# Performance work log

Hardware: AMD Instinct MI355X
Metric: run time of the kernel (lower is better)

The kernel has to match this reference:

```python
import jax, jax.numpy as jnp
import numpy as np

B, C, T = 8, 256, 16000
N_HALF = 32  # d_state // 2 complex modes (S4D stores conjugate pairs)
EPS = 1e-8


def setup_inputs() -> dict:
    key = jax.random.key(0)
    ks = jax.random.split(key, 8)
    x = jax.random.normal(ks[0], (B, C, T), jnp.float32)
    # ChannelwiseLayerNorm params
    gamma = jnp.ones((C,), jnp.float32)
    beta = jnp.zeros((C,), jnp.float32)
    # PReLU per-channel slope (torch default init 0.25)
    prelu_w = jnp.full((C,), 0.25, jnp.float32)
    # S4D kernel params (standard S4D init)
    log_dt = (jax.random.uniform(ks[1], (C,), jnp.float32)
              * (np.log(0.1) - np.log(0.001)) + np.log(0.001)).astype(jnp.float32)
    log_A_real = jnp.log(0.5 * jnp.ones((C, N_HALF), jnp.float32))
    A_imag = jnp.broadcast_to(np.pi * jnp.arange(N_HALF, dtype=jnp.float32), (C, N_HALF))
    C_re = jax.random.normal(ks[2], (C, N_HALF), jnp.float32) * (0.5 ** 0.5)
    C_im = jax.random.normal(ks[3], (C, N_HALF), jnp.float32) * (0.5 ** 0.5)
    D = jax.random.normal(ks[4], (C,), jnp.float32)
    # output 1x1 conv (C -> 2C) followed by GLU over channel dim
    W_out = jax.random.normal(ks[5], (2 * C, C), jnp.float32) * (1.0 / np.sqrt(C))
    b_out = jnp.zeros((2 * C,), jnp.float32)
    return dict(x=x, gamma=gamma, beta=beta, prelu_w=prelu_w, log_dt=log_dt,
                log_A_real=log_A_real, A_imag=A_imag, C_re=C_re, C_im=C_im,
                D=D, W_out=W_out, b_out=b_out)


def reference(x, gamma, beta, prelu_w, log_dt, log_A_real, A_imag, C_re, C_im, D, W_out, b_out):
    # --- channel-wise LayerNorm over C (per timestep), x: [B, C, T] ---
    mean = jnp.mean(x, axis=1, keepdims=True)
    var = jnp.mean((x - mean) ** 2, axis=1, keepdims=True)
    y = (x - mean) * jax.lax.rsqrt(var + EPS)
    y = y * gamma[None, :, None] + beta[None, :, None]
    # --- PReLU (per-channel slope) ---
    y = jnp.where(y >= 0, y, prelu_w[None, :, None] * y)
    # --- S4D convolution kernel via Vandermonde (ZOH discretization) ---
    L = x.shape[-1]
    dt = jnp.exp(log_dt)[:, None]                      # [C, 1]
    A = -jnp.exp(log_A_real) + 1j * A_imag             # [C, N]
    dtA = dt * A                                       # [C, N]
    Cc = (C_re + 1j * C_im) * (jnp.exp(dtA) - 1.0) / A  # [C, N]
    vand = jnp.exp(dtA[:, :, None] * jnp.arange(L))    # [C, N, L]
    k = 2.0 * jnp.real(jnp.einsum('hn,hnl->hl', Cc, vand))  # [C, L]
    # --- FFT-based causal convolution ---
    n = 2 * L
    y_f = jnp.fft.rfft(y, n=n)                         # [B, C, n/2+1]
    k_f = jnp.fft.rfft(k, n=n)                         # [C, n/2+1]
    s = jnp.fft.irfft(y_f * k_f[None], n=n)[..., :L]   # [B, C, T]
    s = s + y * D[None, :, None]                       # skip connection
    # --- GELU + 1x1 conv + GLU over channels ---
    s = jax.nn.gelu(s, approximate=False)
    z = jnp.einsum('bct,oc->bot', s, W_out) + b_out[None, :, None]  # [B, 2C, T]
    out = z[:, :C] * jax.nn.sigmoid(z[:, C:])
    # --- residual ---
    return x + out
```

## Files before the change

### kernel.cpp

```cpp
#include <hip/hip_runtime.h>
#include <cstdint>
#include <cstddef>

constexpr int cB = 8, cC = 256, cT = 16000, cN = 32;
constexpr int cP = 125;
constexpr float cEPS = 1e-8f;

typedef __bf16 bf16;
typedef __bf16 bf16x4 __attribute__((ext_vector_type(4)));
typedef __bf16 bf16x8 __attribute__((ext_vector_type(8)));
typedef float floatx4 __attribute__((ext_vector_type(4)));

constexpr size_t kMean = 0;
constexpr size_t kRstd = kMean + (size_t)cB * cT * 4;
constexpr size_t kWlr  = kRstd + (size_t)cB * cT * 4;
constexpr size_t kWli  = kWlr + (size_t)cC * cN * 4;
constexpr size_t kWb   = kWli + (size_t)cC * cN * 4;
constexpr size_t kLt   = kWb  + (size_t)512 * 256 * 2;
constexpr size_t kEt   = kLt  + (size_t)cC * 128 * 128 * 2;
constexpr size_t kVt   = kEt  + (size_t)cC * 64 * 128 * 2;
constexpr size_t kU    = kVt  + (size_t)cC * 128 * 64 * 2;

__device__ __forceinline__ float fast_sigmoid(float z) {
  return __builtin_amdgcn_rcpf(1.f + __builtin_amdgcn_exp2f(-z * 1.4426950408889634f));
}

__global__ void prepW_kernel(const float* __restrict__ W_out, bf16* __restrict__ Wb) {
  int idx = blockIdx.x * 256 + threadIdx.x;
  if (idx < 512 * 256) Wb[idx] = (bf16)W_out[idx];
}

__global__ void prep2_kernel(const float* __restrict__ log_dt,
                             const float* __restrict__ log_A_real,
                             const float* __restrict__ A_imag,
                             const float* __restrict__ C_re,
                             const float* __restrict__ C_im,
                             float* __restrict__ wlr, float* __restrict__ wli,
                             bf16* __restrict__ Lt, bf16* __restrict__ Et,
                             bf16* __restrict__ Vt) {
  int c = blockIdx.x;
  int j = threadIdx.x;
  __shared__ float kv[128];
  float dt = expf(log_dt[c]);
  float kj = 0.f;
  for (int n = 0; n < cN; ++n) {
    int idx = c * cN + n;
    float Ar = -expf(log_A_real[idx]);
    float Ai = A_imag[idx];
    float ar = dt * Ar, ai = dt * Ai;
    float mg = expf(ar), cw, sw;
    sincosf(ai, &sw, &cw);
    float wre = mg * cw, wim = mg * sw;
    float den = Ar * Ar + Ai * Ai;
    float emr = wre - 1.f, emi = wim;
    float qr = (emr * Ar + emi * Ai) / den;
    float qi = (emi * Ar - emr * Ai) / den;
    float cre = C_re[idx], cim = C_im[idx];
    float c2r = 2.f * (cre * qr - cim * qi);
    float c2i = 2.f * (cre * qi + cim * qr);
    float mj = expf((float)j * ar), cj, sj;
    sincosf((float)j * ai, &sj, &cj);
    float wjr = mj * cj, wji = mj * sj;
    kj += c2r * wjr - c2i * wji;
    float w1r = wjr * wre - wji * wim;
    float w1i = wjr * wim + wji * wre;
    Vt[(size_t)c * 8192 + j * 64 + 2 * n]     = (bf16)(c2r * w1r - c2i * w1i);
    Vt[(size_t)c * 8192 + j * 64 + 2 * n + 1] = (bf16)(-(c2r * w1i + c2i * w1r));
    float mr = expf((float)(127 - j) * ar), cr2, sr2;
    sincosf((float)(127 - j) * ai, &sr2, &cr2);
    Et[(size_t)c * 8192 + (2 * n) * 128 + j]     = (bf16)(mr * cr2);
    Et[(size_t)c * 8192 + (2 * n + 1) * 128 + j] = (bf16)(mr * sr2);
  }
  kv[j] = kj;
  if (j < cN) {
    int idx = c * cN + j;
    float Ar = -expf(log_A_real[idx]);
    float ai = dt * A_imag[idx], ar = dt * Ar;
    float m = expf(128.f * ar), cc, ss;
    sincosf(128.f * ai, &ss, &cc);
    wlr[idx] = m * cc;
    wli[idx] = m * ss;
  }
  __syncthreads();
  bf16* LtC = Lt + (size_t)c * 16384;
  for (int e = j; e < 4096; e += 128) {
    int t4 = e * 4;
    int row = t4 >> 7, col = t4 & 127;
    bf16x4 v;
#pragma unroll
    for (int q = 0; q < 4; ++q) {
      int ii = col + q;
      v[q] = (ii <= row) ? (bf16)kv[row - ii] : (bf16)0.f;
    }
    *(bf16x4*)(LtC + row * 128 + col) = v;
  }
}

__global__ __launch_bounds__(512)
void stats_kernel(const float* __restrict__ x,
                  float* __restrict__ meanp, float* __restrict__ rstdp) {
  __shared__ float S1[8][128], S2[8][128];
  int g0 = blockIdx.x * 128;
  int b = g0 / cT;
  int t0 = g0 - b * cT;
  int tp = threadIdx.x & 63, cq = threadIdx.x >> 6;
  const float2* xp = (const float2*)(x + ((size_t)b * cC + cq * 32) * cT + t0) + tp;
  float s1x = 0.f, s1y = 0.f, s2x = 0.f, s2y = 0.f;
#pragma unroll 8
  for (int cc = 0; cc < 32; ++cc) {
    float2 v = xp[(size_t)cc * (cT / 2)];
    s1x += v.x; s2x = fmaf(v.x, v.x, s2x);
    s1y += v.y; s2y = fmaf(v.y, v.y, s2y);
  }
  S1[cq][2 * tp] = s1x; S1[cq][2 * tp + 1] = s1y;
  S2[cq][2 * tp] = s2x; S2[cq][2 * tp + 1] = s2y;
  __syncthreads();
  if (threadIdx.x < 128) {
    float a1 = 0.f, a2 = 0.f;
#pragma unroll
    for (int q = 0; q < 8; ++q) { a1 += S1[q][threadIdx.x]; a2 += S2[q][threadIdx.x]; }
    float mean = a1 * (1.0f / cC);
    float var = fmaf(a2, 1.0f / cC, -mean * mean);
    int g = g0 + threadIdx.x;
    meanp[g] = mean;
    rstdp[g] = rsqrtf(var + cEPS);
  }
}

__global__ __launch_bounds__(512, 4)
void scanM_kernel(const float* __restrict__ x, const float* __restrict__ meanp,
                  const float* __restrict__ rstdp, const float* __restrict__ gam,
                  const float* __restrict__ bet, const float* __restrict__ prw,
                  const float* __restrict__ Dp,
                  const float* __restrict__ wlr, const float* __restrict__ wli,
                  const bf16* __restrict__ Lt, const bf16* __restrict__ Et,
                  const bf16* __restrict__ Vt, bf16* __restrict__ U) {
  __shared__ __align__(16) bf16 Y[128 * 136];
  __shared__ __align__(16) bf16 H[128 * 136];
  __shared__ float Sseg[8][32][2];

  int blk = blockIdx.x;
  int logical = (blk & 7) * 256 + (blk >> 3);
  int b = logical & 7, c = logical >> 3;
  int tid = threadIdx.x;
  int lane = tid & 63, w8 = tid >> 6, quad = lane >> 4, mh = lane & 15;
  float gamma = gam[c], beta = bet[c], pw = prw[c], Dc = Dp[c];

  const float4* x4 = (const float4*)(x + (size_t)(b * cC + c) * cT);
  const float4* m4 = (const float4*)(meanp + (size_t)b * cT);
  const float4* r4 = (const float4*)(rstdp + (size_t)b * cT);
#pragma unroll
  for (int it = 0; it < 8; ++it) {
    int i4 = tid + it * 512;
    if (i4 < 4000) {
      float4 xv = x4[i4], mv = m4[i4], rv = r4[i4];
      int t = i4 * 4, p = t >> 7, j = t & 127;
      float ys[4];
      ys[0] = fmaf((xv.x - mv.x) * rv.x, gamma, beta);
      ys[1] = fmaf((xv.y - mv.y) * rv.y, gamma, beta);
      ys[2] = fmaf((xv.z - mv.z) * rv.z, gamma, beta);
      ys[3] = fmaf((xv.w - mv.w) * rv.w, gamma, beta);
      bf16x4 yv;
#pragma unroll
      for (int q = 0; q < 4; ++q) {
        float y = ys[q];
        yv[q] = (bf16)(y >= 0.f ? y : y * pw);
      }
      *(bf16x4*)&Y[p * 136 + j] = yv;
    }
  }
  for (int e = tid; e < 3 * 136; e += 512) Y[125 * 136 + e] = (bf16)0.f;
  __syncthreads();

  const bf16* EtC = Et + (size_t)c * 8192;
  int cgrp = (w8 & 3) * 16, mbase = (w8 >> 2) * 4;
  floatx4 hacc[4];
#pragma unroll
  for (int mi = 0; mi < 4; ++mi) hacc[mi] = (floatx4){0.f, 0.f, 0.f, 0.f};
#pragma unroll
  for (int kk = 0; kk < 4; ++kk) {
    bf16x8 bfrag = *(const bf16x8*)(EtC + (cgrp + mh) * 128 + kk * 32 + quad * 8);
#pragma unroll
    for (int mi = 0; mi < 4; ++mi) {
      bf16x8 af = *(bf16x8*)&Y[((mbase + mi) * 16 + mh) * 136 + kk * 32 + quad * 8];
      hacc[mi] = __builtin_amdgcn_mfma_f32_16x16x32_bf16(af, bfrag, hacc[mi], 0, 0, 0);
    }
  }
#pragma unroll
  for (int mi = 0; mi < 4; ++mi) {
#pragma unroll
    for (int r = 0; r < 4; ++r) {
      int p = (mbase + mi) * 16 + quad * 4 + r;
      int comp = cgrp + mh;
      float v = hacc[mi][r];
      bf16 hi = (bf16)v;
      bf16 lo = (bf16)(v - (float)hi);
      H[p * 136 + comp] = hi;
      H[p * 136 + 64 + comp] = lo;
    }
  }
  __syncthreads();

  {
    int n = tid & 31, sg = (tid >> 5) & 7;
    int p0 = sg * 16;
    int p1 = (p0 + 16 < cP) ? p0 + 16 : cP;
    float wr = wlr[c * cN + n], wi = wli[c * cN + n];
    float hR = 0.f, hI = 0.f;
    if (tid < 256) {
      for (int p = p0; p < p1; ++p) {
        float sr = (float)H[p * 136 + 2 * n] + (float)H[p * 136 + 64 + 2 * n];
        float si = (float)H[p * 136 + 2 * n + 1] + (float)H[p * 136 + 64 + 2 * n + 1];
        float t1 = fmaf(wr, hR, fmaf(-wi, hI, sr));
        hI = fmaf(wr, hI, fmaf(wi, hR, si));
        hR = t1;
      }
      Sseg[sg][n][0] = hR; Sseg[sg][n][1] = hI;
    }
    __syncthreads();
    if (tid < 32) {
      float ar = wr, ai = wi;
      for (int q = 0; q < 4; ++q) {
        float nr = ar * ar - ai * ai;
        ai = 2.f * ar * ai; ar = nr;
      }
      float HR = 0.f, HI = 0.f;
      for (int s2 = 0; s2 < 8; ++s2) {
        float fr = Sseg[s2][n][0], fi = Sseg[s2][n][1];
        Sseg[s2][n][0] = HR; Sseg[s2][n][1] = HI;
        float t1 = fmaf(ar, HR, fmaf(-ai, HI, fr));
        HI = fmaf(ar, HI, fmaf(ai, HR, fi));
        HR = t1;
      }
    }
    __syncthreads();
    if (tid < 256) {
      hR = Sseg[sg][n][0]; hI = Sseg[sg][n][1];
      for (int p = p0; p < p1; ++p) {
        float sr = (float)H[p * 136 + 2 * n] + (float)H[p * 136 + 64 + 2 * n];
        float si = (float)H[p * 136 + 2 * n + 1] + (float)H[p * 136 + 64 + 2 * n + 1];
        bf16 hiR = (bf16)hR; bf16 loR = (bf16)(hR - (float)hiR);
        bf16 hiI = (bf16)hI; bf16 loI = (bf16)(hI - (float)hiI);
        H[p * 136 + 2 * n] = hiR;      H[p * 136 + 2 * n + 1] = hiI;
        H[p * 136 + 64 + 2 * n] = loR; H[p * 136 + 64 + 2 * n + 1] = loI;
        float t1 = fmaf(wr, hR, fmaf(-wi, hI, sr));
        hI = fmaf(wr, hI, fmaf(wi, hR, si));
        hR = t1;
      }
    }
  }
  __syncthreads();

  const bf16* LtC = Lt + (size_t)c * 16384;
  const bf16* VtC = Vt + (size_t)c * 8192;
  floatx4 acc[8];
#pragma unroll
  for (int mi = 0; mi < 8; ++mi) acc[mi] = (floatx4){0.f, 0.f, 0.f, 0.f};
#pragma unroll
  for (int kk = 0; kk < 4; ++kk) {
    bf16x8 b0 = *(const bf16x8*)(LtC + (w8 * 16 + mh) * 128 + kk * 32 + quad * 8);
#pragma unroll
    for (int mi = 0; mi < 8; ++mi) {
      bf16x8 af = *(bf16x8*)&Y[(mi * 16 + mh) * 136 + kk * 32 + quad * 8];
      acc[mi] = __builtin_amdgcn_mfma_f32_16x16x32_bf16(af, b0, acc[mi], 0, 0, 0);
    }
  }
#pragma unroll
  for (int kk = 0; kk < 2; ++kk) {
    bf16x8 v0 = *(const bf16x8*)(VtC + (w8 * 16 + mh) * 64 + kk * 32 + quad * 8);
#pragma unroll
    for (int mi = 0; mi < 8; ++mi) {
      bf16x8 ah = *(bf16x8*)&H[(mi * 16 + mh) * 136 + kk * 32 + quad * 8];
      bf16x8 al = *(bf16x8*)&H[(mi * 16 + mh) * 136 + 64 + kk * 32 + quad * 8];
      acc[mi] = __builtin_amdgcn_mfma_f32_16x16x32_bf16(ah, v0, acc[mi], 0, 0, 0);
      acc[mi] = __builtin_amdgcn_mfma_f32_16x16x32_bf16(al, v0, acc[mi], 0, 0, 0);
    }
  }
  bf16 ub[8][4];
  int jcol = w8 * 16 + mh;
#pragma unroll
  for (int mi = 0; mi < 8; ++mi)
#pragma unroll
    for (int r = 0; r < 4; ++r) {
      int p = mi * 16 + quad * 4 + r;
      float y = (float)Y[p * 136 + jcol];
      float sv = fmaf(Dc, y, acc[mi][r]);
      float s3 = sv * sv * sv;
      float zz = 0.7978845608028654f * fmaf(0.044715f, s3, sv);
      float e = __builtin_amdgcn_exp2f(zz * 2.8853900817779268f);
      float th = 1.f - 2.f * __builtin_amdgcn_rcpf(e + 1.f);
      ub[mi][r] = (bf16)(0.5f * sv * (1.f + th));
    }
  __syncthreads();
#pragma unroll
  for (int mi = 0; mi < 8; ++mi)
#pragma unroll
    for (int r = 0; r < 4; ++r) {
      int p = mi * 16 + quad * 4 + r;
      Y[p * 136 + jcol] = ub[mi][r];
    }
  __syncthreads();
  bf16* Uc = U + (size_t)(b * cC + c) * cT;
#pragma unroll
  for (int it = 0; it < 8; ++it) {
    int i4 = tid + it * 512;
    if (i4 < 4000) {
      int t = i4 * 4, p = t >> 7, j = t & 127;
      *(bf16x4*)(Uc + t) = *(bf16x4*)&Y[p * 136 + j];
    }
  }
}

__global__ __launch_bounds__(512, 4)
void gemm2_kernel(const bf16* __restrict__ U, const bf16* __restrict__ Wb,
                  const float* __restrict__ b_out, const float* __restrict__ x,
                  float* __restrict__ out) {
  __shared__ __align__(16) bf16 Ut[64 * 264];
  int bx = blockIdx.x;
  int tb = bx % 250, b = bx / 250;
  int t0 = tb * 64;
  int tid = threadIdx.x, lane = tid & 63, w = tid >> 6, quad = lane >> 4, mh = lane & 15;
  {
    int c = tid & 255, th = tid >> 8;
    const bf16* src = U + (size_t)(b * cC + c) * cT + t0 + th * 32;
#pragma unroll
    for (int g = 0; g < 4; ++g) {
      bf16x8 v = *(const bf16x8*)(src + g * 8);
#pragma unroll
      for (int k = 0; k < 8; ++k) Ut[(th * 32 + g * 8 + k) * 264 + c] = v[k];
    }
  }
  __syncthreads();
  floatx4 a1[2][4], a2[2][4];
#pragma unroll
  for (int oj = 0; oj < 2; ++oj)
#pragma unroll
    for (int tt = 0; tt < 4; ++tt) {
      a1[oj][tt] = (floatx4){0.f, 0.f, 0.f, 0.f};
      a2[oj][tt] = (floatx4){0.f, 0.f, 0.f, 0.f};
    }
#pragma unroll
  for (int kk = 0; kk < 8; ++kk) {
    int ko = kk * 32 + quad * 8;
    bf16x8 wf1[2], wf2[2];
#pragma unroll
    for (int oj = 0; oj < 2; ++oj) {
      int o = w * 32 + oj * 16 + mh;
      wf1[oj] = *(const bf16x8*)(Wb + (size_t)o * 256 + ko);
      wf2[oj] = *(const bf16x8*)(Wb + (size_t)(o + 256) * 256 + ko);
    }
#pragma unroll
    for (int tt = 0; tt < 4; ++tt) {
      bf16x8 uf = *(bf16x8*)&Ut[(tt * 16 + mh) * 264 + ko];
#pragma unroll
      for (int oj = 0; oj < 2; ++oj) {
        a1[oj][tt] = __builtin_amdgcn_mfma_f32_16x16x32_bf16(wf1[oj], uf, a1[oj][tt], 0, 0, 0);
        a2[oj][tt] = __builtin_amdgcn_mfma_f32_16x16x32_bf16(wf2[oj], uf, a2[oj][tt], 0, 0, 0);
      }
    }
  }
#pragma unroll
  for (int oj = 0; oj < 2; ++oj)
#pragma unroll
    for (int tt = 0; tt < 4; ++tt)
#pragma unroll
      for (int r = 0; r < 4; ++r) {
        int o = w * 32 + oj * 16 + quad * 4 + r;
        int t = t0 + tt * 16 + mh;
        float z1 = a1[oj][tt][r] + b_out[o];
        float z2 = a2[oj][tt][r] + b_out[o + 256];
        float sg = fast_sigmoid(z2);
        size_t idx = (size_t)(b * cC + o) * cT + t;
        out[idx] = x[idx] + z1 * sg;
      }
}

extern "C" void kernel_launch(void* const* d_in, const int* in_sizes, int n_in,
                              void* d_out, int out_size, void* d_ws, size_t ws_size,
                              hipStream_t stream) {
  const float* x          = (const float*)d_in[0];
  const float* gamma      = (const float*)d_in[1];
  const float* beta       = (const float*)d_in[2];
  const float* prelu_w    = (const float*)d_in[3];
  const float* log_dt     = (const float*)d_in[4];
  const float* log_A_real = (const float*)d_in[5];
  const float* A_imag     = (const float*)d_in[6];
  const float* C_re       = (const float*)d_in[7];
  const float* C_im       = (const float*)d_in[8];
  const float* Dp         = (const float*)d_in[9];
  const float* W_out      = (const float*)d_in[10];
  const float* b_out      = (const float*)d_in[11];
  float* out = (float*)d_out;
  char* ws = (char*)d_ws;

  float* meanp = (float*)(ws + kMean);
  float* rstdp = (float*)(ws + kRstd);
  float* wlr   = (float*)(ws + kWlr);
  float* wli   = (float*)(ws + kWli);
  bf16*  Wb    = (bf16*)(ws + kWb);
  bf16*  Lt    = (bf16*)(ws + kLt);
  bf16*  Et    = (bf16*)(ws + kEt);
  bf16*  Vt    = (bf16*)(ws + kVt);
  bf16*  U     = (bf16*)(ws + kU);

  prepW_kernel<<<512, 256, 0, stream>>>(W_out, Wb);
  prep2_kernel<<<256, 128, 0, stream>>>(log_dt, log_A_real, A_imag, C_re, C_im,
                                        wlr, wli, Lt, Et, Vt);
  stats_kernel<<<(cB * cT) / 128, 512, 0, stream>>>(x, meanp, rstdp);
  scanM_kernel<<<cB * cC, 512, 0, stream>>>(x, meanp, rstdp, gamma, beta, prelu_w,
                                            Dp, wlr, wli, Lt, Et, Vt, U);
  gemm2_kernel<<<cB * (cT / 64), 512, 0, stream>>>(U, Wb, b_out, x, out);
}
```

Measured before the change: 458.7 us.

## Make gemm2 persistent over four tiles with double-buffered LDS prefetch

The output GEMM+GLU kernel now launches 500 blocks, each handling four 64-timestep tiles in a loop. The next tile's U slice is prefetched into registers while the current tile's MFMAs and epilogue run, then written into an alternate LDS buffer. This is meant to hide global load latency and cut block launch overhead. In exchange LDS use doubles, which can lower occupancy, and the grid has fewer blocks.

```diff
diff --git a/kernel.cpp b/kernel.cpp
--- a/kernel.cpp
+++ b/kernel.cpp
@@ -315,64 +315,92 @@
 void gemm2_kernel(const bf16* __restrict__ U, const bf16* __restrict__ Wb,
                   const float* __restrict__ b_out, const float* __restrict__ x,
                   float* __restrict__ out) {
-  __shared__ __align__(16) bf16 Ut[64 * 264];
-  int bx = blockIdx.x;
-  int tb = bx % 250, b = bx / 250;
-  int t0 = tb * 64;
+  __shared__ __align__(16) bf16 Ut[2][64 * 264];
+  constexpr int NBLK = 500;
   int tid = threadIdx.x, lane = tid & 63, w = tid >> 6, quad = lane >> 4, mh = lane & 15;
+  int cs = tid & 255, th = tid >> 8;
+
+  bf16x8 pre[4];
   {
-    int c = tid & 255, th = tid >> 8;
-    const bf16* src = U + (size_t)(b * cC + c) * cT + t0 + th * 32;
+    int tile = blockIdx.x;
+    int tb = tile % 250, b = tile / 250;
+    const bf16* src = U + (size_t)(b * cC + cs) * cT + tb * 64 + th * 32;
+#pragma unroll
+    for (int g = 0; g < 4; ++g) pre[g] = *(const bf16x8*)(src + g * 8);
 #pragma unroll
     for (int g = 0; g < 4; ++g) {
-      bf16x8 v = *(const bf16x8*)(src + g * 8);
-#pragma unroll
-      for (int k = 0; k < 8; ++k) Ut[(th * 32 + g * 8 + k) * 264 + c] = v[k];
-    }
-  }
-  __syncthreads();
-  floatx4 a1[2][4], a2[2][4];
-#pragma unroll
-  for (int oj = 0; oj < 2; ++oj)
-#pragma unroll
-    for (int tt = 0; tt < 4; ++tt) {
-      a1[oj][tt] = (floatx4){0.f, 0.f, 0.f, 0.f};
-      a2[oj][tt] = (floatx4){0.f, 0.f, 0.f, 0.f};
-    }
-#pragma unroll
-  for (int kk = 0; kk < 8; ++kk) {
-    int ko = kk * 32 + quad * 8;
-    bf16x8 wf1[2], wf2[2];
-#pragma unroll
-    for (int oj = 0; oj < 2; ++oj) {
-      int o = w * 32 + oj * 16 + mh;
-      wf1[oj] = *(const bf16x8*)(Wb + (size_t)o * 256 + ko);
-      wf2[oj] = *(const bf16x8*)(Wb + (size_t)(o + 256) * 256 + ko);
-    }
-#pragma unroll
-    for (int tt = 0; tt < 4; ++tt) {
-      bf16x8 uf = *(bf16x8*)&Ut[(tt * 16 + mh) * 264 + ko];
+      bf16x8 v = pre[g];
+#pragma unroll
+      for (int k = 0; k < 8; ++k) Ut[0][(th * 32 + g * 8 + k) * 264 + cs] = v[k];
+    }
+  }
+  __syncthreads();
+
+#pragma unroll 1
+  for (int i = 0; i < 4; ++i) {
+    int buf = i & 1;
+    int tile = blockIdx.x + i * NBLK;
+    int tb = tile % 250, b = tile / 250;
+    int t0 = tb * 64;
+    if (i < 3) {
+      int ntile = tile + NBLK;
+      int ntb = ntile % 250, nb = ntile / 250;
+      const bf16* src = U + (size_t)(nb * cC + cs) * cT + ntb * 64 + th * 32;
+#pragma unroll
+      for (int g = 0; g < 4; ++g) pre[g] = *(const bf16x8*)(src + g * 8);
+    }
+    floatx4 a1[2][4], a2[2][4];
+#pragma unroll
+    for (int oj = 0; oj < 2; ++oj)
+#pragma unroll
+      for (int tt = 0; tt < 4; ++tt) {
+        a1[oj][tt] = (floatx4){0.f, 0.f, 0.f, 0.f};
+        a2[oj][tt] = (floatx4){0.f, 0.f, 0.f, 0.f};
+      }
+#pragma unroll
+    for (int kk = 0; kk < 8; ++kk) {
+      int ko = kk * 32 + quad * 8;
+      bf16x8 wf1[2], wf2[2];
 #pragma unroll
       for (int oj = 0; oj < 2; ++oj) {
-        a1[oj][tt] = __builtin_amdgcn_mfma_f32_16x16x32_bf16(wf1[oj], uf, a1[oj][tt], 0, 0, 0);
-        a2[oj][tt] = __builtin_amdgcn_mfma_f32_16x16x32_bf16(wf2[oj], uf, a2[oj][tt], 0, 0, 0);
-      }
-    }
-  }
-#pragma unroll
-  for (int oj = 0; oj < 2; ++oj)
-#pragma unroll
-    for (int tt = 0; tt < 4; ++tt)
-#pragma unroll
-      for (int r = 0; r < 4; ++r) {
-        int o = w * 32 + oj * 16 + quad * 4 + r;
-        int t = t0 + tt * 16 + mh;
-        float z1 = a1[oj][tt][r] + b_out[o];
-        float z2 = a2[oj][tt][r] + b_out[o + 256];
-        float sg = fast_sigmoid(z2);
-        size_t idx = (size_t)(b * cC + o) * cT + t;
-        out[idx] = x[idx] + z1 * sg;
-      }
+        int o = w * 32 + oj * 16 + mh;
+        wf1[oj] = *(const bf16x8*)(Wb + (size_t)o * 256 + ko);
+        wf2[oj] = *(const bf16x8*)(Wb + (size_t)(o + 256) * 256 + ko);
+      }
+#pragma unroll
+      for (int tt = 0; tt < 4; ++tt) {
+        bf16x8 uf = *(bf16x8*)&Ut[buf][(tt * 16 + mh) * 264 + ko];
+#pragma unroll
+        for (int oj = 0; oj < 2; ++oj) {
+          a1[oj][tt] = __builtin_amdgcn_mfma_f32_16x16x32_bf16(wf1[oj], uf, a1[oj][tt], 0, 0, 0);
+          a2[oj][tt] = __builtin_amdgcn_mfma_f32_16x16x32_bf16(wf2[oj], uf, a2[oj][tt], 0, 0, 0);
+        }
+      }
+    }
+#pragma unroll
+    for (int oj = 0; oj < 2; ++oj)
+#pragma unroll
+      for (int tt = 0; tt < 4; ++tt)
+#pragma unroll
+        for (int r = 0; r < 4; ++r) {
+          int o = w * 32 + oj * 16 + quad * 4 + r;
+          int t = t0 + tt * 16 + mh;
+          float z1 = a1[oj][tt][r] + b_out[o];
+          float z2 = a2[oj][tt][r] + b_out[o + 256];
+          float sg = fast_sigmoid(z2);
+          size_t idx = (size_t)(b * cC + o) * cT + t;
+          out[idx] = x[idx] + z1 * sg;
+        }
+    if (i < 3) {
+#pragma unroll
+      for (int g = 0; g < 4; ++g) {
+        bf16x8 v = pre[g];
+#pragma unroll
+        for (int k = 0; k < 8; ++k) Ut[buf ^ 1][(th * 32 + g * 8 + k) * 264 + cs] = v[k];
+      }
+      __syncthreads();
+    }
+  }
 }
 
 extern "C" void kernel_launch(void* const* d_in, const int* in_sizes, int n_in,
@@ -409,5 +437,5 @@
   stats_kernel<<<(cB * cT) / 128, 512, 0, stream>>>(x, meanp, rstdp);
   scanM_kernel<<<cB * cC, 512, 0, stream>>>(x, meanp, rstdp, gamma, beta, prelu_w,
                                             Dp, wlr, wli, Lt, Et, Vt, U);
-  gemm2_kernel<<<cB * (cT / 64), 512, 0, stream>>>(U, Wb, b_out, x, out);
-}
+  gemm2_kernel<<<500, 512, 0, stream>>>(U, Wb, b_out, x, out);
+}
```

Result: slower. 587.6 us (+28.1%).
